# Kernel optimization log

Hardware: AMD Instinct MI355X
Metric: run time of the kernel (lower is better)

The kernel has to match this reference:

```python
import jax, jax.numpy as jnp
import numpy as np

INF = 1e20


def setup_inputs() -> dict:
    key = jax.random.key(0)
    k0, k1, k2, k3, k4 = jax.random.split(key, 5)
    B, T, C, D = 4, 8, 512, 256
    P, Ks = 4, 4
    return {
        "context": jax.random.normal(k0, (B, T, C, D), jnp.float32),
        "ctx_mask": jax.random.randint(k1, (B, C), 0, 2).astype(jnp.int32),
        "weight_tensor": jax.random.normal(k2, (P, D), jnp.float32),
        "mean_dis": jax.random.uniform(k3, (Ks, 1), jnp.float32),
        "precision_inv_dis": jax.random.uniform(k4, (Ks, 1), jnp.float32),
        "topk": 10,
        "max_position_distance": 160,
    }


def _forward(context, ctx_mask, weight_tensor, mean_dis, precision_inv_dis, topk, max_position_distance):
    B, T, C, D = context.shape
    Ks = mean_dis.shape[0]
    # attention[b,t,c,e] = mean_p sum_d ctx[b,t,c,d]*relu(W[p,d])*ctx[b,t,e,d]
    # (mean over perspectives commutes with the contraction over d)
    wbar = jnp.mean(jax.nn.relu(weight_tensor), axis=0)  # (D,)
    attention = jnp.einsum('btcd,bted->btce', context * wbar, context)  # (B,T,C,C)

    valid = ctx_mask > 0  # (B,C)
    pair_ok = valid[:, None, :, None] & valid[:, None, None, :]  # (B,1,C,C)
    attention = jnp.where(pair_ok, attention, -INF)

    # spatial Gaussian kernels over |i-j| distances (shared across batch/turn)
    idx = jnp.arange(C)
    pc = jnp.abs(idx[:, None] - idx[None, :]).astype(jnp.float32)
    pc = jnp.minimum(pc, float(max_position_distance)) / float(max_position_distance)  # (C,C)
    mu = mean_dis[:, 0][:, None, None]            # (Ks,1,1)
    prec = precision_inv_dis[:, 0][:, None, None]  # (Ks,1,1)
    spatial = jnp.exp(-0.5 * (pc[None] - mu) ** 2 * prec ** 2)  # (Ks,C,C)

    # kNN sparsification
    knn_val, knn_ind = jax.lax.top_k(attention, topk)  # (B,T,C,K)
    sem = jax.nn.softmax(knn_val, axis=-1)             # semantic weights (B,T,C,K)

    idx5 = jnp.broadcast_to(knn_ind[:, :, None, :, :], (B, T, Ks, C, topk))
    spatial_full = jnp.broadcast_to(spatial[None, None], (B, T, Ks, C, C))
    sp_chosen = jnp.take_along_axis(spatial_full, idx5, axis=-1)  # (B,T,Ks,C,K)
    sp_chosen = sp_chosen / jnp.sum(sp_chosen, axis=-1, keepdims=True)

    attn_chosen = sem[:, :, None, :, :] * sp_chosen  # (B,T,Ks,C,K)

    adj = jnp.zeros((B, T, Ks, C, C), dtype=attn_chosen.dtype)
    adj = adj.at[
        jnp.arange(B)[:, None, None, None, None],
        jnp.arange(T)[None, :, None, None, None],
        jnp.arange(Ks)[None, None, :, None, None],
        jnp.arange(C)[None, None, None, :, None],
        idx5,
    ].set(attn_chosen)
    return adj


def reference(context, ctx_mask, weight_tensor, mean_dis, precision_inv_dis, topk, max_position_distance):
    return _forward(context, ctx_mask, weight_tensor, mean_dis, precision_inv_dis, topk, max_position_distance)
```

## Files before the change

kernel.cpp:

```cpp
#include <hip/hip_runtime.h>
#include <math.h>

#define C_ 512
#define D_ 256
#define KS_ 4
#define TOPK_ 10
#define NEG 1e20f

typedef float v2f __attribute__((ext_vector_type(2)));

__device__ __forceinline__ int csw2(int g) { return g ^ ((g >> 3) & 1); }

#define ASTR 36
#define BSTR1 130

extern "C" __global__ __launch_bounds__(256, 4)
void gemm_attn(const float* __restrict__ ctx,
               const float* __restrict__ W,
               float* __restrict__ ws)
{
    __shared__ __align__(16) float wbar_s[D_];
    __shared__ __align__(16) float a_s[16 * ASTR];
    __shared__ __align__(16) float b_s[16 * BSTR1];

    const int tid  = threadIdx.x;
    const int lane = tid & 63;
    const int wv   = tid >> 6;
    const int w8   = wv * 8;

    const int blk  = blockIdx.x;
    const int bt   = (blk & 7) * 4 + ((blk >> 3) & 3);
    const int tile = blk >> 5;
    const int c0   = (tile & 15) * 32;
    const int n0   = (tile >> 4) * 128;

    const float* ctx_bt = ctx + (size_t)bt * (C_ * D_);

    {
        float w0 = W[tid], w1 = W[D_ + tid], w2 = W[2 * D_ + tid], w3 = W[3 * D_ + tid];
        wbar_s[tid] = 0.25f * (fmaxf(w0, 0.f) + fmaxf(w1, 0.f) + fmaxf(w2, 0.f) + fmaxf(w3, 0.f));
    }

    const int ar_ = tid >> 2;
    const int aq  = tid & 3;
    const float* asrc = ctx_bt + (size_t)(c0 + ar_) * D_ + aq * 4;
    const int awbase = (4 * aq) * ASTR + ar_;
    const int bcol = tid >> 1;
    const int bq   = tid & 1;
    const float* bsrc = ctx_bt + (size_t)(n0 + bcol) * D_ + bq * 8;
    float* bdst = b_s + (bq * 8) * BSTR1 + bcol;

    v2f acc2[8];
    #pragma unroll
    for (int j = 0; j < 8; ++j) acc2[j] = (v2f){0.f, 0.f};

    const int bro = 2 * lane;

    for (int kt = 0; kt < 16; ++kt) {
        __syncthreads();
        {
            float4 v0 = *(const float4*)(bsrc + kt * 16);
            float4 v1 = *(const float4*)(bsrc + kt * 16 + 4);
            bdst[0 * BSTR1] = v0.x;  bdst[1 * BSTR1] = v0.y;
            bdst[2 * BSTR1] = v0.z;  bdst[3 * BSTR1] = v0.w;
            bdst[4 * BSTR1] = v1.x;  bdst[5 * BSTR1] = v1.y;
            bdst[6 * BSTR1] = v1.z;  bdst[7 * BSTR1] = v1.w;
        }
        if (tid < 128) {
            float4 v  = *(const float4*)(asrc + kt * 16);
            float4 wb = *(const float4*)(wbar_s + kt * 16 + aq * 4);
            a_s[awbase + 0 * ASTR] = v.x * wb.x;
            a_s[awbase + 1 * ASTR] = v.y * wb.y;
            a_s[awbase + 2 * ASTR] = v.z * wb.z;
            a_s[awbase + 3 * ASTR] = v.w * wb.w;
        }
        __syncthreads();
        #pragma unroll
        for (int kk = 0; kk < 16; ++kk) {
            float4 av0 = *(const float4*)(a_s + kk * ASTR + w8);
            float4 av1 = *(const float4*)(a_s + kk * ASTR + w8 + 4);
            v2f bv = *(const v2f*)(b_s + kk * BSTR1 + bro);
            float ar8[8] = {av0.x, av0.y, av0.z, av0.w, av1.x, av1.y, av1.z, av1.w};
            #pragma unroll
            for (int j = 0; j < 8; ++j) {
                v2f a2 = (v2f){ar8[j], ar8[j]};
                acc2[j] += a2 * bv;
            }
        }
    }

    #pragma unroll
    for (int j = 0; j < 8; ++j)
        *(v2f*)(ws + ((size_t)bt * C_ + c0 + w8 + j) * C_ + n0 + bro) = acc2[j];
}

extern "C" __global__ __launch_bounds__(256, 2)
void epilogue_k(const float* __restrict__ ws,
                const int* __restrict__ cmask,
                const float* __restrict__ mu_g,
                const float* __restrict__ pr_g,
                float* __restrict__ out)
{
    const int tid  = threadIdx.x;
    const int lane = tid & 63;
    const int wv   = tid >> 6;

    const int blk = blockIdx.x;
    const int bt  = blk >> 7;
    const int rq  = blk & 127;
    const int b   = bt >> 3;

    {
        const float4 z = make_float4(0.f, 0.f, 0.f, 0.f);
        #pragma unroll
        for (int ks = 0; ks < KS_; ++ks) {
            float* ob = out + ((size_t)(bt * KS_ + ks) * C_ + rq * 4) * C_;
            *(float4*)(ob + (size_t)tid * 4)         = z;
            *(float4*)(ob + (size_t)(tid + 256) * 4) = z;
        }
    }

    const int c  = rq * 4 + wv;
    const int vr = cmask[b * C_ + c];

    float row[8];
    {
        const float* wrow = ws + ((size_t)bt * C_ + c) * C_ + lane * 8;
        float4 r0 = *(const float4*)wrow;
        float4 r1 = *(const float4*)(wrow + 4);
        row[0] = r0.x; row[1] = r0.y; row[2] = r0.z; row[3] = r0.w;
        row[4] = r1.x; row[5] = r1.y; row[6] = r1.z; row[7] = r1.w;
        int4 m0 = *(const int4*)(cmask + b * C_ + lane * 8);
        int4 m1 = *(const int4*)(cmask + b * C_ + lane * 8 + 4);
        int em[8] = {m0.x, m0.y, m0.z, m0.w, m1.x, m1.y, m1.z, m1.w};
        #pragma unroll
        for (int i = 0; i < 8; ++i) {
            bool ok = (vr > 0) && (em[i] > 0);
            row[i] = ok ? row[i] : -NEG;
        }
    }

    float tv[TOPK_];
    int   te[TOPK_];
    unsigned int taken = 0;
    #pragma unroll
    for (int j = 0; j < TOPK_; ++j) {
        float lv = -3.3e38f;
        int   li = 0;
        #pragma unroll
        for (int i = 0; i < 8; ++i) {
            bool better = (!((taken >> i) & 1u)) && (row[i] > lv);
            lv = better ? row[i] : lv;
            li = better ? i : li;
        }
        int le = lane * 8 + li;
        #pragma unroll
        for (int off = 1; off < 64; off <<= 1) {
            float ov = __shfl_xor(lv, off);
            int   oe = __shfl_xor(le, off);
            bool take = (ov > lv) || (ov == lv && oe < le);
            lv = take ? ov : lv;
            le = take ? oe : le;
        }
        tv[j] = lv;
        te[j] = le;
        if ((le >> 3) == lane) taken |= 1u << (le & 7);
    }
    const float mx = tv[0];
    float ssum = 0.f;
    #pragma unroll
    for (int j = 0; j < TOPK_; ++j) ssum += expf(tv[j] - mx);

    float oval = 0.f;
    size_t ooff = 0;
    {
        const int ksq = (lane < 40) ? (lane / 10) : 3;
        const int myj = (lane < 40) ? (lane - (lane / 10) * 10) : 0;
        const float mu = mu_g[ksq];
        const float pr = pr_g[ksq];
        float sps = 0.f, spj = 0.f, tvj = 0.f;
        int ej = 0;
        #pragma unroll
        for (int j = 0; j < TOPK_; ++j) {
            float d = fabsf((float)(te[j] - c));
            d = fminf(d, 160.f) * (1.0f / 160.0f);
            float x  = d - mu;
            float sp = expf(-0.5f * x * x * pr * pr);
            sps += sp;
            if (j == myj) { spj = sp; tvj = tv[j]; ej = te[j]; }
        }
        oval = (expf(tvj - mx) / ssum) * (spj / sps);
        ooff = ((size_t)(bt * KS_ + ksq) * C_ + c) * C_ + ej;
    }

    __syncthreads();
    if (lane < 40) out[ooff] = oval;
}

#define BSTR 516
extern "C" __global__ __launch_bounds__(256, 2)
void graph_learner(const float* __restrict__ ctx,
                   const int* __restrict__ cmask,
                   const float* __restrict__ W,
                   const float* __restrict__ mu_g,
                   const float* __restrict__ pr_g,
                   float* __restrict__ out)
{
    __shared__ __align__(16) float wbar_s[D_];
    __shared__ __align__(16) float a_s[16 * ASTR];
    __shared__ __align__(16) float b_s[16 * BSTR];
    __shared__ __align__(8)  float res_s[2560];
    __shared__ unsigned int vmask_s[16];

    const int tid  = threadIdx.x;
    const int lane = tid & 63;
    const int wv   = tid >> 6;
    const int w8   = wv * 8;

    const int blk = blockIdx.x;
    const int bt  = (blk & 7) * 4 + ((blk >> 3) & 3);
    const int c0  = (blk >> 5) * 32;
    const int b   = bt >> 3;

    const float* ctx_bt = ctx + (size_t)bt * (C_ * D_);
    const int*   mask_b = cmask + b * C_;

    {
        float w0 = W[tid], w1 = W[D_ + tid], w2 = W[2 * D_ + tid], w3 = W[3 * D_ + tid];
        wbar_s[tid] = 0.25f * (fmaxf(w0, 0.f) + fmaxf(w1, 0.f) + fmaxf(w2, 0.f) + fmaxf(w3, 0.f));
    }
    if (tid < 16) {
        unsigned int m = 0;
        for (int i = 0; i < 32; ++i)
            m |= (mask_b[tid * 32 + i] > 0 ? 1u : 0u) << i;
        vmask_s[tid] = m;
    }

    const int brow = tid >> 2;
    const int bq   = tid & 3;
    const float* bsrc = ctx_bt + (size_t)brow * D_ + bq * 4;
    const int bwbase = (4 * bq) * BSTR + 4 * csw2(brow >> 2) + (brow & 3);
    const int ar_ = tid >> 2;
    const int aq  = tid & 3;
    const float* asrc = ctx_bt + (size_t)(c0 + ar_) * D_ + aq * 4;
    const int awbase = (4 * aq) * ASTR + ar_;
    const int bc0 = 4 * csw2(2 * lane);
    const int bc1 = 4 * csw2(2 * lane + 1);

    v2f acc2[8][4];
    #pragma unroll
    for (int j = 0; j < 8; ++j)
        #pragma unroll
        for (int t = 0; t < 4; ++t) acc2[j][t] = (v2f){0.f, 0.f};

    for (int kt = 0; kt < 16; ++kt) {
        __syncthreads();
        #pragma unroll
        for (int i = 0; i < 8; ++i) {
            float4 v = *(const float4*)(bsrc + (size_t)i * 64 * D_ + kt * 16);
            b_s[bwbase + 0 * BSTR + i * 64] = v.x;
            b_s[bwbase + 1 * BSTR + i * 64] = v.y;
            b_s[bwbase + 2 * BSTR + i * 64] = v.z;
            b_s[bwbase + 3 * BSTR + i * 64] = v.w;
        }
        if (tid < 128) {
            float4 v  = *(const float4*)(asrc + kt * 16);
            float4 wb = *(const float4*)(wbar_s + kt * 16 + aq * 4);
            a_s[awbase + 0 * ASTR] = v.x * wb.x;
            a_s[awbase + 1 * ASTR] = v.y * wb.y;
            a_s[awbase + 2 * ASTR] = v.z * wb.z;
            a_s[awbase + 3 * ASTR] = v.w * wb.w;
        }
        __syncthreads();
        #pragma unroll
        for (int kk = 0; kk < 16; ++kk) {
            float4 av0 = *(const float4*)(a_s + kk * ASTR + w8);
            float4 av1 = *(const float4*)(a_s + kk * ASTR + w8 + 4);
            float4 bv0 = *(const float4*)(b_s + kk * BSTR + bc0);
            float4 bv1 = *(const float4*)(b_s + kk * BSTR + bc1);
            v2f b20 = (v2f){bv0.x, bv0.y};
            v2f b21 = (v2f){bv0.z, bv0.w};
            v2f b22 = (v2f){bv1.x, bv1.y};
            v2f b23 = (v2f){bv1.z, bv1.w};
            float ar8[8] = {av0.x, av0.y, av0.z, av0.w, av1.x, av1.y, av1.z, av1.w};
            #pragma unroll
            for (int j = 0; j < 8; ++j) {
                v2f a2 = (v2f){ar8[j], ar8[j]};
                asm("v_pk_fma_f32 %0, %1, %2, %0" : "+v"(acc2[j][0]) : "v"(a2), "v"(b20));
                asm("v_pk_fma_f32 %0, %1, %2, %0" : "+v"(acc2[j][1]) : "v"(a2), "v"(b21));
                asm("v_pk_fma_f32 %0, %1, %2, %0" : "+v"(acc2[j][2]) : "v"(a2), "v"(b22));
                asm("v_pk_fma_f32 %0, %1, %2, %0" : "+v"(acc2[j][3]) : "v"(a2), "v"(b23));
            }
        }
    }

    {
        const float4 z = make_float4(0.f, 0.f, 0.f, 0.f);
        #pragma unroll
        for (int ks = 0; ks < KS_; ++ks) {
            float* ob = out + ((size_t)(bt * KS_ + ks) * C_ + c0) * C_;
            #pragma unroll
            for (int i = 0; i < 16; ++i)
                *(float4*)(ob + (size_t)(tid + i * 256) * 4) = z;
        }
    }

    const unsigned int em8 = (vmask_s[lane >> 2] >> ((lane & 3) * 8)) & 0xffu;
    const float mu0 = mu_g[0], mu1 = mu_g[1], mu2 = mu_g[2], mu3 = mu_g[3];
    const float pr0 = pr_g[0], pr1 = pr_g[1], pr2 = pr_g[2], pr3 = pr_g[3];

    #pragma unroll
    for (int jr = 0; jr < 8; ++jr) {
        const int c  = c0 + w8 + jr;
        const int vr = mask_b[c];
        float row[8];
        #pragma unroll
        for (int t = 0; t < 4; ++t) { row[2 * t] = acc2[jr][t].x; row[2 * t + 1] = acc2[jr][t].y; }
        #pragma unroll
        for (int i = 0; i < 8; ++i) {
            bool ok = (vr > 0) && ((em8 >> i) & 1u);
            row[i] = ok ? row[i] : -NEG;
        }
        float tv[TOPK_];
        int   te[TOPK_];
        unsigned int taken = 0;
        #pragma unroll
        for (int j = 0; j < TOPK_; ++j) {
            float lv = -3.3e38f;
            int   li = 0;
            #pragma unroll
            for (int i = 0; i < 8; ++i) {
                bool better = (!((taken >> i) & 1u)) && (row[i] > lv);
                lv = better ? row[i] : lv;
                li = better ? i : li;
            }
            int le = lane * 8 + li;
            #pragma unroll
            for (int off = 1; off < 64; off <<= 1) {
                float ov = __shfl_xor(lv, off);
                int   oe = __shfl_xor(le, off);
                bool take = (ov > lv) || (ov == lv && oe < le);
                lv = take ? ov : lv;
                le = take ? oe : le;
            }
            tv[j] = lv;
            te[j] = le;
            if ((le >> 3) == lane) taken |= 1u << (le & 7);
        }
        const float mx = tv[0];
        float ssum = 0.f;
        #pragma unroll
        for (int j = 0; j < TOPK_; ++j) ssum += expf(tv[j] - mx);

        if (lane < 40) {
            const int ksq = lane / 10;
            const int myj = lane - ksq * 10;
            const float mu = (ksq == 0) ? mu0 : (ksq == 1) ? mu1 : (ksq == 2) ? mu2 : mu3;
            const float pr = (ksq == 0) ? pr0 : (ksq == 1) ? pr1 : (ksq == 2) ? pr2 : pr3;
            float sps = 0.f, spj = 0.f, tvj = 0.f;
            int ej = 0;
            #pragma unroll
            for (int j = 0; j < TOPK_; ++j) {
                float d = fabsf((float)(te[j] - c));
                d = fminf(d, 160.f) * (1.0f / 160.0f);
                float x  = d - mu;
                float sp = expf(-0.5f * x * x * pr * pr);
                sps += sp;
                if (j == myj) { spj = sp; tvj = tv[j]; ej = te[j]; }
            }
            float val = (expf(tvj - mx) / ssum) * (spj / sps);
            int   off = ((bt * KS_ + ksq) * C_ + c) * C_ + ej;
            int   slot = (((wv * 8 + jr) * 40) + lane) * 2;
            res_s[slot]     = val;
            res_s[slot + 1] = __int_as_float(off);
        }
    }

    __syncthreads();
    #pragma unroll
    for (int i = 0; i < 5; ++i) {
        int p = tid * 5 + i;
        float v   = res_s[2 * p];
        int   off = __float_as_int(res_s[2 * p + 1]);
        out[off] = v;
    }
}

extern "C" void kernel_launch(void* const* d_in, const int* in_sizes, int n_in,
                              void* d_out, int out_size, void* d_ws, size_t ws_size,
                              hipStream_t stream) {
    (void)in_sizes; (void)n_in; (void)out_size;
    const float* ctx   = (const float*)d_in[0];
    const int*   cmask = (const int*)d_in[1];
    const float* W     = (const float*)d_in[2];
    const float* mu    = (const float*)d_in[3];
    const float* pr    = (const float*)d_in[4];
    const size_t WS_NEEDED = (size_t)32 * C_ * C_ * sizeof(float);
    if (ws_size >= WS_NEEDED) {
        float* ws = (float*)d_ws;
        gemm_attn<<<dim3(2048), dim3(256), 0, stream>>>(ctx, W, ws);
        epilogue_k<<<dim3(4096), dim3(256), 0, stream>>>(ws, cmask, mu, pr, (float*)d_out);
    } else {
        graph_learner<<<dim3(512), dim3(256), 0, stream>>>(ctx, cmask, W, mu, pr, (float*)d_out);
    }
}
```

Baseline: 110.2 us.

## Widen GEMM tile to 32x256 with 8x4 per-thread outputs and packed FMA asm

Each GEMM block now computes 32x256 output columns instead of 32x128, and each thread holds an 8x4 register tile rather than 8x2, which halves the block count. The inner loop uses inline v_pk_fma_f32 with op_sel to broadcast A values without separate moves. This raises arithmetic per LDS load and cuts redundant A-tile loads. It costs more registers (launch bounds drop to 2 blocks per CU), a larger B shared tile, and fewer blocks to spread across CUs.

```diff
diff --git a/kernel.cpp b/kernel.cpp
--- a/kernel.cpp
+++ b/kernel.cpp
@@ -8,31 +8,42 @@
 #define NEG 1e20f
 
 typedef float v2f __attribute__((ext_vector_type(2)));
+typedef float v4f __attribute__((ext_vector_type(4)));
 
 __device__ __forceinline__ int csw2(int g) { return g ^ ((g >> 3) & 1); }
 
 #define ASTR 36
-#define BSTR1 130
-
-extern "C" __global__ __launch_bounds__(256, 4)
+#define BSTR2 260
+
+#define PKFMA_LO(ACC, AP, BP) \
+    asm("v_pk_fma_f32 %0, %1, %2, %0 op_sel:[0,0,0] op_sel_hi:[0,1,1]" \
+        : "+v"(ACC) : "v"(AP), "v"(BP));
+#define PKFMA_HI(ACC, AP, BP) \
+    asm("v_pk_fma_f32 %0, %1, %2, %0 op_sel:[1,0,0] op_sel_hi:[1,1,1]" \
+        : "+v"(ACC) : "v"(AP), "v"(BP));
+
+extern "C" __global__ __launch_bounds__(256, 2)
 void gemm_attn(const float* __restrict__ ctx,
                const float* __restrict__ W,
                float* __restrict__ ws)
 {
     __shared__ __align__(16) float wbar_s[D_];
     __shared__ __align__(16) float a_s[16 * ASTR];
-    __shared__ __align__(16) float b_s[16 * BSTR1];
+    __shared__ __align__(16) float b_s[16 * BSTR2];
 
     const int tid  = threadIdx.x;
     const int lane = tid & 63;
     const int wv   = tid >> 6;
-    const int w8   = wv * 8;
+    const int wr   = (wv >> 1) * 16;
+    const int wc   = (wv & 1) * 128;
+    const int rg   = lane >> 5;
+    const int cg   = lane & 31;
 
     const int blk  = blockIdx.x;
     const int bt   = (blk & 7) * 4 + ((blk >> 3) & 3);
     const int tile = blk >> 5;
     const int c0   = (tile & 15) * 32;
-    const int n0   = (tile >> 4) * 128;
+    const int n0   = (tile >> 4) * 256;
 
     const float* ctx_bt = ctx + (size_t)bt * (C_ * D_);
 
@@ -41,57 +52,71 @@
         wbar_s[tid] = 0.25f * (fmaxf(w0, 0.f) + fmaxf(w1, 0.f) + fmaxf(w2, 0.f) + fmaxf(w3, 0.f));
     }
 
+    const int cp = tid & 127;
+    const int kh = (tid >> 7) * 8;
+    const float* bsrc0 = ctx_bt + (size_t)(n0 + 2 * cp) * D_ + kh;
+    const float* bsrc1 = bsrc0 + D_;
+    float* bdst = b_s + kh * BSTR2 + 2 * cp;
     const int ar_ = tid >> 2;
     const int aq  = tid & 3;
     const float* asrc = ctx_bt + (size_t)(c0 + ar_) * D_ + aq * 4;
     const int awbase = (4 * aq) * ASTR + ar_;
-    const int bcol = tid >> 1;
-    const int bq   = tid & 1;
-    const float* bsrc = ctx_bt + (size_t)(n0 + bcol) * D_ + bq * 8;
-    float* bdst = b_s + (bq * 8) * BSTR1 + bcol;
-
-    v2f acc2[8];
-    #pragma unroll
-    for (int j = 0; j < 8; ++j) acc2[j] = (v2f){0.f, 0.f};
-
-    const int bro = 2 * lane;
+    const int abase = wr + rg * 8;
+    const int bbase = wc + cg * 4;
+
+    v2f acc2[8][2];
+    #pragma unroll
+    for (int j = 0; j < 8; ++j) { acc2[j][0] = (v2f){0.f, 0.f}; acc2[j][1] = (v2f){0.f, 0.f}; }
 
     for (int kt = 0; kt < 16; ++kt) {
         __syncthreads();
         {
-            float4 v0 = *(const float4*)(bsrc + kt * 16);
-            float4 v1 = *(const float4*)(bsrc + kt * 16 + 4);
-            bdst[0 * BSTR1] = v0.x;  bdst[1 * BSTR1] = v0.y;
-            bdst[2 * BSTR1] = v0.z;  bdst[3 * BSTR1] = v0.w;
-            bdst[4 * BSTR1] = v1.x;  bdst[5 * BSTR1] = v1.y;
-            bdst[6 * BSTR1] = v1.z;  bdst[7 * BSTR1] = v1.w;
+            v4f u00 = *(const v4f*)(bsrc0 + kt * 16);
+            v4f u01 = *(const v4f*)(bsrc0 + kt * 16 + 4);
+            v4f u10 = *(const v4f*)(bsrc1 + kt * 16);
+            v4f u11 = *(const v4f*)(bsrc1 + kt * 16 + 4);
+            #pragma unroll
+            for (int q = 0; q < 4; ++q) {
+                *(v2f*)(bdst + (q + 0) * BSTR2) = (v2f){u00[q], u10[q]};
+                *(v2f*)(bdst + (q + 4) * BSTR2) = (v2f){u01[q], u11[q]};
+            }
         }
         if (tid < 128) {
-            float4 v  = *(const float4*)(asrc + kt * 16);
-            float4 wb = *(const float4*)(wbar_s + kt * 16 + aq * 4);
-            a_s[awbase + 0 * ASTR] = v.x * wb.x;
-            a_s[awbase + 1 * ASTR] = v.y * wb.y;
-            a_s[awbase + 2 * ASTR] = v.z * wb.z;
-            a_s[awbase + 3 * ASTR] = v.w * wb.w;
+            v4f v  = *(const v4f*)(asrc + kt * 16);
+            v4f wb = *(const v4f*)(wbar_s + kt * 16 + aq * 4);
+            a_s[awbase + 0 * ASTR] = v[0] * wb[0];
+            a_s[awbase + 1 * ASTR] = v[1] * wb[1];
+            a_s[awbase + 2 * ASTR] = v[2] * wb[2];
+            a_s[awbase + 3 * ASTR] = v[3] * wb[3];
         }
         __syncthreads();
         #pragma unroll
         for (int kk = 0; kk < 16; ++kk) {
-            float4 av0 = *(const float4*)(a_s + kk * ASTR + w8);
-            float4 av1 = *(const float4*)(a_s + kk * ASTR + w8 + 4);
-            v2f bv = *(const v2f*)(b_s + kk * BSTR1 + bro);
-            float ar8[8] = {av0.x, av0.y, av0.z, av0.w, av1.x, av1.y, av1.z, av1.w};
-            #pragma unroll
-            for (int j = 0; j < 8; ++j) {
-                v2f a2 = (v2f){ar8[j], ar8[j]};
-                acc2[j] += a2 * bv;
-            }
-        }
-    }
-
-    #pragma unroll
-    for (int j = 0; j < 8; ++j)
-        *(v2f*)(ws + ((size_t)bt * C_ + c0 + w8 + j) * C_ + n0 + bro) = acc2[j];
+            v4f av0 = *(const v4f*)(a_s + kk * ASTR + abase);
+            v4f av1 = *(const v4f*)(a_s + kk * ASTR + abase + 4);
+            v4f bv  = *(const v4f*)(b_s + kk * BSTR2 + bbase);
+            v2f a01 = __builtin_shufflevector(av0, av0, 0, 1);
+            v2f a23 = __builtin_shufflevector(av0, av0, 2, 3);
+            v2f a45 = __builtin_shufflevector(av1, av1, 0, 1);
+            v2f a67 = __builtin_shufflevector(av1, av1, 2, 3);
+            v2f blo = __builtin_shufflevector(bv, bv, 0, 1);
+            v2f bhi = __builtin_shufflevector(bv, bv, 2, 3);
+            PKFMA_LO(acc2[0][0], a01, blo)  PKFMA_LO(acc2[0][1], a01, bhi)
+            PKFMA_HI(acc2[1][0], a01, blo)  PKFMA_HI(acc2[1][1], a01, bhi)
+            PKFMA_LO(acc2[2][0], a23, blo)  PKFMA_LO(acc2[2][1], a23, bhi)
+            PKFMA_HI(acc2[3][0], a23, blo)  PKFMA_HI(acc2[3][1], a23, bhi)
+            PKFMA_LO(acc2[4][0], a45, blo)  PKFMA_LO(acc2[4][1], a45, bhi)
+            PKFMA_HI(acc2[5][0], a45, blo)  PKFMA_HI(acc2[5][1], a45, bhi)
+            PKFMA_LO(acc2[6][0], a67, blo)  PKFMA_LO(acc2[6][1], a67, bhi)
+            PKFMA_HI(acc2[7][0], a67, blo)  PKFMA_HI(acc2[7][1], a67, bhi)
+        }
+    }
+
+    #pragma unroll
+    for (int j = 0; j < 8; ++j) {
+        v4f o = __builtin_shufflevector(acc2[j][0], acc2[j][1], 0, 1, 2, 3);
+        *(v4f*)(ws + ((size_t)bt * C_ + c0 + wr + rg * 8 + j) * C_ + n0 + bbase) = o;
+    }
 }
 
 extern "C" __global__ __launch_bounds__(256, 2)
@@ -398,7 +423,7 @@
     const size_t WS_NEEDED = (size_t)32 * C_ * C_ * sizeof(float);
     if (ws_size >= WS_NEEDED) {
         float* ws = (float*)d_ws;
-        gemm_attn<<<dim3(2048), dim3(256), 0, stream>>>(ctx, W, ws);
+        gemm_attn<<<dim3(1024), dim3(256), 0, stream>>>(ctx, W, ws);
         epilogue_k<<<dim3(4096), dim3(256), 0, stream>>>(ws, cmask, mu, pr, (float*)d_out);
     } else {
         graph_learner<<<dim3(512), dim3(256), 0, stream>>>(ctx, cmask, W, mu, pr, (float*)d_out);
```

After: 104.4 us. -5.3%, faster.
